# Kernel tuning notes

Hardware: AMD Instinct MI355X
Metric: run time of the kernel (lower is better)

The kernel has to match this reference:

```python
import jax, jax.numpy as jnp
import numpy as np

HEADS = 8
DIM_HEAD = 64
QUERY_DIM = 512
CONTEXT_DIM = 768
INNER_DIM = HEADS * DIM_HEAD  # 512
SCALE = DIM_HEAD ** -0.5


def setup_inputs() -> dict:
    key = jax.random.key(0)
    ks = jax.random.split(key, 7)
    B, N, M = 4, 2048, 1024
    x = jax.random.normal(ks[0], (B, N, QUERY_DIM), dtype=jnp.float32)
    context = jax.random.normal(ks[1], (B, M, CONTEXT_DIM), dtype=jnp.float32)
    # torch Linear weights stored as (out_features, in_features); y = x @ W.T
    Wq = jax.random.normal(ks[2], (INNER_DIM, QUERY_DIM), dtype=jnp.float32) * (QUERY_DIM ** -0.5)
    Wk = jax.random.normal(ks[3], (INNER_DIM, CONTEXT_DIM), dtype=jnp.float32) * (CONTEXT_DIM ** -0.5)
    Wv = jax.random.normal(ks[4], (INNER_DIM, CONTEXT_DIM), dtype=jnp.float32) * (CONTEXT_DIM ** -0.5)
    Wo = jax.random.normal(ks[5], (QUERY_DIM, INNER_DIM), dtype=jnp.float32) * (INNER_DIM ** -0.5)
    bo = jax.random.normal(ks[6], (QUERY_DIM,), dtype=jnp.float32) * 0.01
    return {"x": x, "context": context, "Wq": Wq, "Wk": Wk, "Wv": Wv, "Wo": Wo, "bo": bo}


def reference(x, context, Wq, Wk, Wv, Wo, bo):
    B, N, _ = x.shape
    M = context.shape[1]
    h, d = HEADS, DIM_HEAD
    q = jnp.einsum('bnc,ic->bni', x, Wq)        # [B,N,inner]
    k = jnp.einsum('bmc,ic->bmi', context, Wk)  # [B,M,inner]
    v = jnp.einsum('bmc,ic->bmi', context, Wv)  # [B,M,inner]
    # split heads: b n (h d) -> b h n d
    q = q.reshape(B, N, h, d).transpose(0, 2, 1, 3)
    k = k.reshape(B, M, h, d).transpose(0, 2, 1, 3)
    v = v.reshape(B, M, h, d).transpose(0, 2, 1, 3)
    # fp32 upcast for QK^T (inputs already fp32; kept explicit for fidelity)
    sim = jnp.einsum('bhnd,bhmd->bhnm', q.astype(jnp.float32), k.astype(jnp.float32)) * SCALE
    attn = jax.nn.softmax(sim, axis=-1)
    out = jnp.einsum('bhnm,bhmd->bhnd', attn, v)  # [B,h,N,d]
    out = out.transpose(0, 2, 1, 3).reshape(B, N, h * d)  # b n (h d)
    return jnp.einsum('bni,oi->bno', out, Wo) + bo  # dropout p=0 in eval
```

## Files before the change

### kernel.cpp

```cpp
#include <hip/hip_runtime.h>

using u16 = unsigned short;
typedef __bf16 bf16x8 __attribute__((ext_vector_type(8)));
typedef __bf16 bf16x2 __attribute__((ext_vector_type(2)));
typedef float  f32x4  __attribute__((ext_vector_type(4)));
typedef float  f32x16 __attribute__((ext_vector_type(16)));

#define MFMA16x16x32 __builtin_amdgcn_mfma_f32_16x16x32_bf16
#define MFMA32x32x16 __builtin_amdgcn_mfma_f32_32x32x16_bf16

#if __has_builtin(__builtin_amdgcn_exp2f)
#define EXP2 __builtin_amdgcn_exp2f
#else
#define EXP2 exp2f
#endif

static __device__ __forceinline__ unsigned f2bf_u(float f){
  unsigned x = __builtin_bit_cast(unsigned, f);
  return (x + 0x7fffu + ((x >> 16) & 1u)) >> 16;
}

static __device__ __forceinline__ void gll16(const void* g, void* l){
  __builtin_amdgcn_global_load_lds((const __attribute__((address_space(1))) void*)g,
                                   (__attribute__((address_space(3))) void*)l, 16, 0, 0);
}

static __device__ __forceinline__ f32x16 splat16(float x){
  f32x16 v;
#pragma unroll
  for (int i = 0; i < 16; ++i) v[i] = x;
  return v;
}

__global__ void __launch_bounds__(256) cvt_all(
    const float* __restrict__ x,  u16* __restrict__ xb,
    const float* __restrict__ cx, u16* __restrict__ cxb,
    const float* __restrict__ wq, u16* __restrict__ wqb,
    const float* __restrict__ wk, u16* __restrict__ wkb,
    const float* __restrict__ wv, u16* __restrict__ wvb,
    const float* __restrict__ wo, u16* __restrict__ wob)
{
  const float* in; u16* out; int n4;
  switch (blockIdx.y){
    case 0: in=x;  out=xb;  n4=(4*2048*512)/4; break;
    case 1: in=cx; out=cxb; n4=(4*1024*768)/4; break;
    case 2: in=wq; out=wqb; n4=(512*512)/4;    break;
    case 3: in=wk; out=wkb; n4=(512*768)/4;    break;
    case 4: in=wv; out=wvb; n4=(512*768)/4;    break;
    default:in=wo; out=wob; n4=(512*512)/4;    break;
  }
  int i = blockIdx.x*256 + threadIdx.x;
  const int stride = gridDim.x*256;
  for (; i < n4; i += stride){
    float4 f = ((const float4*)in)[i];
    ushort4 u;
    u.x = (u16)f2bf_u(f.x); u.y = (u16)f2bf_u(f.y);
    u.z = (u16)f2bf_u(f.z); u.w = (u16)f2bf_u(f.w);
    ((ushort4*)out)[i] = u;
  }
}

template<int LDA, int LDB, int KK, int OM>
static __device__ __forceinline__ void gemm_tile64(
    const u16* __restrict__ Ap, const u16* __restrict__ Bp,
    void* __restrict__ Cv, int ldc, int bx, int by,
    const float* __restrict__ bias, float scale,
    u16* __restrict__ sAp, u16* __restrict__ sBp)
{
  const int tid = threadIdx.x;
  const int w = tid >> 6, lane = tid & 63;
  const int wr = w >> 1, wc = w & 1;
  const long tm = (long)bx * 128;
  const long tn = (long)by * 64;

  f32x4 acc[4][2] = {};

  const int srl = lane >> 3, scc = lane & 7;

  auto stage = [&](int kt, int bb){
#pragma unroll
    for (int i = 0; i < 4; ++i){
      const int row = w*32 + i*8 + srl;
      const int sw = scc ^ (row & 7);
      gll16(Ap + (tm + row)*LDA + kt*64 + sw*8, sAp + bb*(128*64) + (w*32 + i*8)*64);
    }
#pragma unroll
    for (int i = 0; i < 2; ++i){
      const int row = w*16 + i*8 + srl;
      const int sw = scc ^ (row & 7);
      gll16(Bp + (tn + row)*LDB + kt*64 + sw*8, sBp + bb*(64*64) + (w*16 + i*8)*64);
    }
  };

  const int fr = lane & 15, fg = lane >> 4;
  constexpr int NK = KK / 64;

  stage(0, 0);
  __syncthreads();
  for (int kt = 0; kt < NK; ++kt){
    if (kt + 1 < NK) stage(kt + 1, (kt + 1) & 1);
    const int bb = kt & 1;
    bf16x8 af[4][2], bfr[2][2];
#pragma unroll
    for (int fm = 0; fm < 4; ++fm){
      const int row = wr*64 + fm*16 + fr;
      const int swz = row & 7;
#pragma unroll
      for (int s = 0; s < 2; ++s)
        af[fm][s] = *(const bf16x8*)&sAp[bb*(128*64) + row*64 + ((s*4 + fg) ^ swz)*8];
    }
#pragma unroll
    for (int fn = 0; fn < 2; ++fn){
      const int row = wc*32 + fn*16 + fr;
      const int swz = row & 7;
#pragma unroll
      for (int s = 0; s < 2; ++s)
        bfr[fn][s] = *(const bf16x8*)&sBp[bb*(64*64) + row*64 + ((s*4 + fg) ^ swz)*8];
    }
#pragma unroll
    for (int s = 0; s < 2; ++s)
#pragma unroll
      for (int fm = 0; fm < 4; ++fm)
#pragma unroll
        for (int fn = 0; fn < 2; ++fn)
          acc[fm][fn] = MFMA16x16x32(af[fm][s], bfr[fn][s], acc[fm][fn], 0, 0, 0);
    __syncthreads();
  }

#pragma unroll
  for (int fm = 0; fm < 4; ++fm){
#pragma unroll
    for (int fn = 0; fn < 2; ++fn){
      const long row0 = tm + wr*64 + fm*16 + fg*4;
      const long col  = tn + wc*32 + fn*16 + fr;
      if (OM == 0){
        u16* C = (u16*)Cv;
#pragma unroll
        for (int rr = 0; rr < 4; ++rr)
          C[(row0 + rr)*ldc + col] = (u16)f2bf_u(acc[fm][fn][rr] * scale);
      } else {
        float* C = (float*)Cv;
        const float bv = bias[col];
#pragma unroll
        for (int rr = 0; rr < 4; ++rr)
          C[(row0 + rr)*ldc + col] = acc[fm][fn][rr] + bv;
      }
    }
  }
}

template<int LDA, int LDB, int KK, int OM>
static __device__ __forceinline__ void gemm_tile128(
    const u16* __restrict__ Ap, const u16* __restrict__ Bp,
    void* __restrict__ Cv, int ldc, int bx, int by,
    const float* __restrict__ bias, float scale,
    u16* __restrict__ sAp, u16* __restrict__ sBp)
{
  const int tid = threadIdx.x;
  const int w = tid >> 6, lane = tid & 63;
  const int wr = w >> 1, wc = w & 1;
  const long tm = (long)bx * 128;
  const long tn = (long)by * 128;

  f32x4 acc[4][4] = {};

  const int srl = lane >> 3, scc = lane & 7;

  auto stage = [&](int kt, int bb){
#pragma unroll
    for (int i = 0; i < 4; ++i){
      const int row = w*32 + i*8 + srl;
      const int sw = scc ^ (row & 7);
      gll16(Ap + (tm + row)*LDA + kt*64 + sw*8, sAp + bb*(128*64) + (w*32 + i*8)*64);
      gll16(Bp + (tn + row)*LDB + kt*64 + sw*8, sBp + bb*(128*64) + (w*32 + i*8)*64);
    }
  };

  const int fr = lane & 15, fg = lane >> 4;
  constexpr int NK = KK / 64;

  stage(0, 0);
  __syncthreads();
  for (int kt = 0; kt < NK; ++kt){
    if (kt + 1 < NK) stage(kt + 1, (kt + 1) & 1);
    const int bb = kt & 1;
    bf16x8 af[4][2], bfr[4][2];
#pragma unroll
    for (int fm = 0; fm < 4; ++fm){
      const int row = wr*64 + fm*16 + fr;
      const int swz = row & 7;
#pragma unroll
      for (int s = 0; s < 2; ++s)
        af[fm][s] = *(const bf16x8*)&sAp[bb*(128*64) + row*64 + ((s*4 + fg) ^ swz)*8];
    }
#pragma unroll
    for (int fn = 0; fn < 4; ++fn){
      const int row = wc*64 + fn*16 + fr;
      const int swz = row & 7;
#pragma unroll
      for (int s = 0; s < 2; ++s)
        bfr[fn][s] = *(const bf16x8*)&sBp[bb*(128*64) + row*64 + ((s*4 + fg) ^ swz)*8];
    }
#pragma unroll
    for (int s = 0; s < 2; ++s)
#pragma unroll
      for (int fm = 0; fm < 4; ++fm)
#pragma unroll
        for (int fn = 0; fn < 4; ++fn)
          acc[fm][fn] = MFMA16x16x32(af[fm][s], bfr[fn][s], acc[fm][fn], 0, 0, 0);
    __syncthreads();
  }

#pragma unroll
  for (int fm = 0; fm < 4; ++fm){
#pragma unroll
    for (int fn = 0; fn < 4; ++fn){
      const long row0 = tm + wr*64 + fm*16 + fg*4;
      const long col  = tn + wc*64 + fn*16 + fr;
      if (OM == 0){
        u16* C = (u16*)Cv;
#pragma unroll
        for (int rr = 0; rr < 4; ++rr)
          C[(row0 + rr)*ldc + col] = (u16)f2bf_u(acc[fm][fn][rr] * scale);
      } else {
        float* C = (float*)Cv;
        const float bv = bias[col];
#pragma unroll
        for (int rr = 0; rr < 4; ++rr)
          C[(row0 + rr)*ldc + col] = acc[fm][fn][rr] + bv;
      }
    }
  }
}

__global__ __launch_bounds__(256, 2) void proj_fused(
    const u16* __restrict__ xb,  const u16* __restrict__ cxb,
    const u16* __restrict__ wqb, const u16* __restrict__ wkb,
    const u16* __restrict__ wvb,
    u16* __restrict__ qb, u16* __restrict__ kb, u16* __restrict__ vtb,
    float qscale)
{
  __shared__ u16 sA[2*128*64];
  __shared__ u16 sB[2*128*64];
  const int bid = blockIdx.x;
  const int lid = (bid & 7)*64 + (bid >> 3);
  if (lid < 256){
    gemm_tile128<512,512,512,0>(xb, wqb, (void*)qb, 512, lid >> 2, lid & 3,
                                nullptr, qscale, sA, sB);
  } else if (lid < 384){
    const int t = lid - 256;
    gemm_tile128<768,768,768,0>(cxb, wkb, (void*)kb, 512, t >> 2, t & 3,
                                nullptr, 1.0f, sA, sB);
  } else {
    const int t = lid - 384, z = t >> 5, r = t & 31;
    gemm_tile128<768,768,768,0>(wvb, cxb + (long)z*1024*768,
                                (void*)(vtb + (long)z*512*1024), 1024,
                                r >> 3, r & 7, nullptr, 1.0f, sA, sB);
  }
}

__global__ __launch_bounds__(256, 3) void gemm_out(
    const u16* __restrict__ ab, const u16* __restrict__ wob,
    float* __restrict__ out, const float* __restrict__ bias)
{
  __shared__ u16 sA[2*128*64];
  __shared__ u16 sB[2*64*64];
  const int bid = blockIdx.x;
  const int lid = (bid & 7)*64 + (bid >> 3);
  gemm_tile64<512,512,512,1>(ab, wob, (void*)out, 512, lid >> 3, lid & 7,
                             bias, 1.0f, sA, sB);
}

__global__ __launch_bounds__(512, 2) void attn_fwd(
    const u16* __restrict__ Q,
    const u16* __restrict__ Kb,
    const u16* __restrict__ Vt,
    u16* __restrict__ O)
{
  const int bid = blockIdx.x;
  const int lid = (bid & 7)*32 + (bid >> 3);
  const int qx = lid & 7, hh = (lid >> 3) & 7, b = lid >> 6;
  const int w = threadIdx.x >> 6, lane = threadIdx.x & 63;
  const int q31 = lane & 31, hi = lane >> 5;
  const int w4 = w & 3, kvg = w >> 2;
  const int q0 = qx*256 + w4*64;

  __shared__ u16 sK[8][64*64];
  __shared__ u16 sV[8][64*64];
  __shared__ float sLsP[16*32];
  __shared__ float sLsT[8*32];

  bf16x8 qf[2][4];
#pragma unroll
  for (int j = 0; j < 2; ++j){
    const u16* qrow = Q + (long)(b*2048 + q0 + j*32 + q31)*512 + hh*64;
#pragma unroll
    for (int ks = 0; ks < 4; ++ks)
      qf[j][ks] = *(const bf16x8*)(qrow + ks*16 + hi*8);
  }

  f32x16 o[2][2] = {{splat16(0.f), splat16(0.f)}, {splat16(0.f), splat16(0.f)}};
  float lsum0 = 0.f, lsum1 = 0.f;

  const int srl = lane >> 3, scc = lane & 7;

  auto stagePair = [&](int u){
    const int tv = 2*u + kvg;
    const int sl = tv & 7;
#pragma unroll
    for (int i = 0; i < 2; ++i){
      const int row = w4*16 + i*8 + srl;
      const int sw = scc ^ (row & 7);
      gll16(Kb + (long)(b*1024 + tv*64 + row)*512 + hh*64 + sw*8,
            &sK[sl][(w4*16 + i*8)*64]);
      gll16(Vt + (long)(b*512 + hh*64 + row)*1024 + tv*64 + sw*8,
            &sV[sl][(w4*16 + i*8)*64]);
    }
  };

  stagePair(0);
  stagePair(1);

  for (int t = 0; t < 8; ++t){
    if (t + 2 < 8) stagePair(t + 2);
    if (t <= 5)      asm volatile("s_waitcnt vmcnt(8)" ::: "memory");
    else if (t == 6) asm volatile("s_waitcnt vmcnt(4)" ::: "memory");
    else             asm volatile("s_waitcnt vmcnt(0)" ::: "memory");
    __builtin_amdgcn_s_barrier();
    asm volatile("" ::: "memory");
    const int tv = 2*t + kvg;
    const int sl = tv & 7;
    const u16* sKp = sK[sl];
    const u16* sVp = sV[sl];

#pragma unroll
    for (int mt = 0; mt < 2; ++mt){
      f32x16 s0 = splat16(-16.f), s1 = splat16(-16.f);
      const int row = mt*32 + q31;
      const int swz = row & 7;
      __builtin_amdgcn_s_setprio(1);
#pragma unroll
      for (int ks = 0; ks < 4; ++ks){
        bf16x8 kf = *(const bf16x8*)&sKp[row*64 + ((ks*2 + hi) ^ swz)*8];
        s0 = MFMA32x32x16(kf, qf[0][ks], s0, 0, 0, 0);
        s1 = MFMA32x32x16(kf, qf[1][ks], s1, 0, 0, 0);
      }
      __builtin_amdgcn_s_setprio(0);

      unsigned pk0[8], pk1[8];
#pragma unroll
      for (int r = 0; r < 16; ++r){ s0[r] = EXP2(s0[r]); lsum0 += s0[r]; }
#pragma unroll
      for (int r = 0; r < 16; ++r){ s1[r] = EXP2(s1[r]); lsum1 += s1[r]; }
#pragma unroll
      for (int p2 = 0; p2 < 8; ++p2){
        union { bf16x2 h; unsigned u; } t0, t1;
        t0.h[0] = (__bf16)s0[2*p2]; t0.h[1] = (__bf16)s0[2*p2 + 1]; pk0[p2] = t0.u;
        t1.h[0] = (__bf16)s1[2*p2]; t1.h[1] = (__bf16)s1[2*p2 + 1]; pk1[p2] = t1.u;
      }

#pragma unroll
      for (int sl2 = 0; sl2 < 2; ++sl2){
        union { unsigned u[4]; bf16x8 v; } pa0, pa1;
        {
          const unsigned ca = pk0[sl2*4 + 0], cb = pk0[sl2*4 + 1];
          const unsigned cc = pk0[sl2*4 + 2], cd = pk0[sl2*4 + 3];
          const unsigned ya = hi ? ca : cc;
          const unsigned za = (unsigned)__shfl_xor((int)ya, 32);
          const unsigned yb = hi ? cb : cd;
          const unsigned zb = (unsigned)__shfl_xor((int)yb, 32);
          pa0.u[0] = hi ? za : ca;
          pa0.u[1] = hi ? zb : cb;
          pa0.u[2] = hi ? cc : za;
          pa0.u[3] = hi ? cd : zb;
        }
        {
          const unsigned ca = pk1[sl2*4 + 0], cb = pk1[sl2*4 + 1];
          const unsigned cc = pk1[sl2*4 + 2], cd = pk1[sl2*4 + 3];
          const unsigned ya = hi ? ca : cc;
          const unsigned za = (unsigned)__shfl_xor((int)ya, 32);
          const unsigned yb = hi ? cb : cd;
          const unsigned zb = (unsigned)__shfl_xor((int)yb, 32);
          pa1.u[0] = hi ? za : ca;
          pa1.u[1] = hi ? zb : cb;
          pa1.u[2] = hi ? cc : za;
          pa1.u[3] = hi ? cd : zb;
        }
        const int s = mt*2 + sl2;
        __builtin_amdgcn_s_setprio(1);
#pragma unroll
        for (int fd = 0; fd < 2; ++fd){
          const int vrow = fd*32 + q31;
          bf16x8 bv = *(const bf16x8*)&sVp[vrow*64 + (((s*2 + hi) ^ (vrow & 7)))*8];
          o[0][fd] = MFMA32x32x16(pa0.v, bv, o[0][fd], 0, 0, 0);
          o[1][fd] = MFMA32x32x16(pa1.v, bv, o[1][fd], 0, 0, 0);
        }
        __builtin_amdgcn_s_setprio(0);
      }
    }
    asm volatile("" ::: "memory");
  }

  lsum0 += __shfl_xor(lsum0, 32);
  lsum1 += __shfl_xor(lsum1, 32);
  sLsP[(w*2 + 0)*32 + q31] = lsum0;
  sLsP[(w*2 + 1)*32 + q31] = lsum1;
  __syncthreads();

  float* sO = (float*)&sK[0][0];
  if (w >= 4){
#pragma unroll
    for (int j = 0; j < 2; ++j){
#pragma unroll
      for (int fd = 0; fd < 2; ++fd){
        float* p = sO + ((((w - 4)*2 + j)*2 + fd)*64*20) + lane*20;
#pragma unroll
        for (int k = 0; k < 4; ++k){
          f32x4 t4;
#pragma unroll
          for (int e = 0; e < 4; ++e) t4[e] = o[j][fd][4*k + e];
          *(f32x4*)(p + 4*k) = t4;
        }
      }
    }
  }
  __syncthreads();

  if (w < 4){
#pragma unroll
    for (int j = 0; j < 2; ++j){
#pragma unroll
      for (int fd = 0; fd < 2; ++fd){
        const float* p = sO + (((w*2 + j)*2 + fd)*64*20) + lane*20;
#pragma unroll
        for (int k = 0; k < 4; ++k){
          f32x4 t4 = *(const f32x4*)(p + 4*k);
#pragma unroll
          for (int e = 0; e < 4; ++e) o[j][fd][4*k + e] += t4[e];
        }
      }
    }
    const float lt0 = lsum0 + sLsP[((w + 4)*2 + 0)*32 + q31];
    const float lt1 = lsum1 + sLsP[((w + 4)*2 + 1)*32 + q31];
    sLsT[(w*2 + 0)*32 + q31] = lt0;
    sLsT[(w*2 + 1)*32 + q31] = lt1;
  }
  __syncthreads();

  if (w < 4){
#pragma unroll
    for (int j = 0; j < 2; ++j){
      f32x4 inv[4];
#pragma unroll
      for (int g = 0; g < 4; ++g){
        f32x4 ls = *(const f32x4*)&sLsT[(w*2 + j)*32 + 8*g + 4*hi];
#pragma unroll
        for (int e = 0; e < 4; ++e) inv[g][e] = 1.0f / ls[e];
      }
      u16* orow = O + (long)(b*2048 + q0 + j*32)*512 + hh*64;
#pragma unroll
      for (int fd = 0; fd < 2; ++fd){
#pragma unroll
        for (int r = 0; r < 16; ++r){
          const int q = (r & 3) + 8*(r >> 2) + 4*hi;
          const float val = o[j][fd][r] * inv[r >> 2][r & 3];
          orow[(long)q*512 + fd*32 + q31] = (u16)f2bf_u(val);
        }
      }
    }
  }
}

extern "C" void kernel_launch(void* const* d_in, const int* in_sizes, int n_in,
                              void* d_out, int out_size, void* d_ws, size_t ws_size,
                              hipStream_t stream)
{
  (void)in_sizes; (void)n_in; (void)out_size; (void)ws_size;
  const float* x   = (const float*)d_in[0];
  const float* ctx = (const float*)d_in[1];
  const float* Wq  = (const float*)d_in[2];
  const float* Wk  = (const float*)d_in[3];
  const float* Wv  = (const float*)d_in[4];
  const float* Wo  = (const float*)d_in[5];
  const float* bo  = (const float*)d_in[6];
  float* out = (float*)d_out;

  char* ws = (char*)d_ws;
  u16* xb  = (u16*)(ws + 0);
  u16* cxb = (u16*)(ws + 8388608);
  u16* wqb = (u16*)(ws + 14680064);
  u16* wkb = (u16*)(ws + 15204352);
  u16* wvb = (u16*)(ws + 15990784);
  u16* wob = (u16*)(ws + 16777216);
  u16* qb  = (u16*)(ws + 17301504);
  u16* kb  = (u16*)(ws + 25690112);
  u16* vtb = (u16*)(ws + 29884416);
  u16* ab  = (u16*)(ws + 34078720);

  cvt_all<<<dim3(1024, 6, 1), 256, 0, stream>>>(x, xb, ctx, cxb, Wq, wqb,
                                                Wk, wkb, Wv, wvb, Wo, wob);

  proj_fused<<<dim3(512, 1, 1), 256, 0, stream>>>(
      xb, cxb, wqb, wkb, wvb, qb, kb, vtb, 0.18033688011112042f);

  attn_fwd<<<dim3(256, 1, 1), 512, 0, stream>>>(qb, kb, vtb, ab);

  gemm_out<<<dim3(512, 1, 1), 256, 0, stream>>>(ab, wob, out, bo);
}
```

Baseline: 67.19 us.

## Halve attention block size to 4 waves with smaller K/V ring and more blocks

The attention kernel now uses 256-thread blocks covering 128 queries instead of 512-thread blocks covering 256, so twice as many blocks are launched. The K/V shared ring shrinks from 128 KB to 64 KB, with whole waves dedicated to loading either K or V. Prefetch depth drops from two tiles ahead to one, with a full vmcnt(0) wait each iteration. The aim is to improve occupancy and CU load balance, at the cost of doubled K/V global traffic across blocks and less latency hiding from the shallower prefetch.

```diff
diff --git a/kernel.cpp b/kernel.cpp
--- a/kernel.cpp
+++ b/kernel.cpp
@@ -271,24 +271,23 @@
                              bias, 1.0f, sA, sB);
 }
 
-__global__ __launch_bounds__(512, 2) void attn_fwd(
+__global__ __launch_bounds__(256, 2) void attn_fwd(
     const u16* __restrict__ Q,
     const u16* __restrict__ Kb,
     const u16* __restrict__ Vt,
     u16* __restrict__ O)
 {
   const int bid = blockIdx.x;
-  const int lid = (bid & 7)*32 + (bid >> 3);
-  const int qx = lid & 7, hh = (lid >> 3) & 7, b = lid >> 6;
+  const int lid = (bid & 7)*64 + (bid >> 3);
+  const int qx = lid & 15, hh = (lid >> 4) & 7, b = lid >> 7;
   const int w = threadIdx.x >> 6, lane = threadIdx.x & 63;
   const int q31 = lane & 31, hi = lane >> 5;
-  const int w4 = w & 3, kvg = w >> 2;
-  const int q0 = qx*256 + w4*64;
-
-  __shared__ u16 sK[8][64*64];
-  __shared__ u16 sV[8][64*64];
-  __shared__ float sLsP[16*32];
-  __shared__ float sLsT[8*32];
+  const int qw = w & 1, kvg = w >> 1;
+  const int q0 = qx*128 + qw*64;
+
+  __shared__ u16 sRing[8][64*64];
+  __shared__ float sLsP[8*32];
+  __shared__ float sLsT[4*32];
 
   bf16x8 qf[2][4];
 #pragma unroll
@@ -305,33 +304,39 @@
   const int srl = lane >> 3, scc = lane & 7;
 
   auto stagePair = [&](int u){
-    const int tv = 2*u + kvg;
-    const int sl = tv & 7;
-#pragma unroll
-    for (int i = 0; i < 2; ++i){
-      const int row = w4*16 + i*8 + srl;
-      const int sw = scc ^ (row & 7);
-      gll16(Kb + (long)(b*1024 + tv*64 + row)*512 + hh*64 + sw*8,
-            &sK[sl][(w4*16 + i*8)*64]);
-      gll16(Vt + (long)(b*512 + hh*64 + row)*1024 + tv*64 + sw*8,
-            &sV[sl][(w4*16 + i*8)*64]);
+    const int tvs = 2*u + (w >> 1);
+    const int sl = tvs & 3;
+    if ((w & 1) == 0){
+#pragma unroll
+      for (int i = 0; i < 8; ++i){
+        const int row = i*8 + srl;
+        const int sw = scc ^ (row & 7);
+        gll16(Kb + (long)(b*1024 + tvs*64 + row)*512 + hh*64 + sw*8,
+              &sRing[sl][(i*8)*64]);
+      }
+    } else {
+#pragma unroll
+      for (int i = 0; i < 8; ++i){
+        const int row = i*8 + srl;
+        const int sw = scc ^ (row & 7);
+        gll16(Vt + (long)(b*512 + hh*64 + row)*1024 + tvs*64 + sw*8,
+              &sRing[4 + sl][(i*8)*64]);
+      }
     }
   };
 
   stagePair(0);
-  stagePair(1);
 
   for (int t = 0; t < 8; ++t){
-    if (t + 2 < 8) stagePair(t + 2);
-    if (t <= 5)      asm volatile("s_waitcnt vmcnt(8)" ::: "memory");
-    else if (t == 6) asm volatile("s_waitcnt vmcnt(4)" ::: "memory");
-    else             asm volatile("s_waitcnt vmcnt(0)" ::: "memory");
+    asm volatile("s_waitcnt vmcnt(0)" ::: "memory");
     __builtin_amdgcn_s_barrier();
     asm volatile("" ::: "memory");
+    if (t + 1 < 8) stagePair(t + 1);
+
     const int tv = 2*t + kvg;
-    const int sl = tv & 7;
-    const u16* sKp = sK[sl];
-    const u16* sVp = sV[sl];
+    const int sl = tv & 3;
+    const u16* sKp = sRing[sl];
+    const u16* sVp = sRing[4 + sl];
 
 #pragma unroll
     for (int mt = 0; mt < 2; ++mt){
@@ -407,13 +412,13 @@
   sLsP[(w*2 + 1)*32 + q31] = lsum1;
   __syncthreads();
 
-  float* sO = (float*)&sK[0][0];
-  if (w >= 4){
+  float* sO = (float*)&sRing[0][0];
+  if (kvg == 1){
 #pragma unroll
     for (int j = 0; j < 2; ++j){
 #pragma unroll
       for (int fd = 0; fd < 2; ++fd){
-        float* p = sO + ((((w - 4)*2 + j)*2 + fd)*64*20) + lane*20;
+        float* p = sO + (((qw*2 + j)*2 + fd)*64*20) + lane*20;
 #pragma unroll
         for (int k = 0; k < 4; ++k){
           f32x4 t4;
@@ -426,12 +431,12 @@
   }
   __syncthreads();
 
-  if (w < 4){
+  if (kvg == 0){
 #pragma unroll
     for (int j = 0; j < 2; ++j){
 #pragma unroll
       for (int fd = 0; fd < 2; ++fd){
-        const float* p = sO + (((w*2 + j)*2 + fd)*64*20) + lane*20;
+        const float* p = sO + (((qw*2 + j)*2 + fd)*64*20) + lane*20;
 #pragma unroll
         for (int k = 0; k < 4; ++k){
           f32x4 t4 = *(const f32x4*)(p + 4*k);
@@ -440,20 +445,20 @@
         }
       }
     }
-    const float lt0 = lsum0 + sLsP[((w + 4)*2 + 0)*32 + q31];
-    const float lt1 = lsum1 + sLsP[((w + 4)*2 + 1)*32 + q31];
-    sLsT[(w*2 + 0)*32 + q31] = lt0;
-    sLsT[(w*2 + 1)*32 + q31] = lt1;
+    const float lt0 = lsum0 + sLsP[((2 + qw)*2 + 0)*32 + q31];
+    const float lt1 = lsum1 + sLsP[((2 + qw)*2 + 1)*32 + q31];
+    sLsT[(qw*2 + 0)*32 + q31] = lt0;
+    sLsT[(qw*2 + 1)*32 + q31] = lt1;
   }
   __syncthreads();
 
-  if (w < 4){
+  if (kvg == 0){
 #pragma unroll
     for (int j = 0; j < 2; ++j){
       f32x4 inv[4];
 #pragma unroll
       for (int g = 0; g < 4; ++g){
-        f32x4 ls = *(const f32x4*)&sLsT[(w*2 + j)*32 + 8*g + 4*hi];
+        f32x4 ls = *(const f32x4*)&sLsT[(qw*2 + j)*32 + 8*g + 4*hi];
 #pragma unroll
         for (int e = 0; e < 4; ++e) inv[g][e] = 1.0f / ls[e];
       }
@@ -503,7 +508,7 @@
   proj_fused<<<dim3(512, 1, 1), 256, 0, stream>>>(
       xb, cxb, wqb, wkb, wvb, qb, kb, vtb, 0.18033688011112042f);
 
-  attn_fwd<<<dim3(256, 1, 1), 512, 0, stream>>>(qb, kb, vtb, ab);
+  attn_fwd<<<dim3(512, 1, 1), 256, 0, stream>>>(qb, kb, vtb, ab);
 
   gemm_out<<<dim3(512, 1, 1), 256, 0, stream>>>(ab, wob, out, bo);
 }
```

Result: slower. 69.27 us (+3.1%).

## Stage 128-row KV tiles with double buffering and permlane32 swap for P

Applied to the files above, without the earlier changes.

Restructures the attention K/V staging from a 3-deep ring of 64-row tiles into double-buffered 128-row tiles (4 iterations instead of 8), with a wider 16-way swizzle for the V tile. The aim is fewer barriers and loop iterations per block. It also replaces the shfl_xor-plus-select exchange of P fragments with v_permlane32_swap, and reduces the row sums as a tree to shorten the dependency chain. The cost is a shallower prefetch with a full vmcnt(0) wait each iteration, so load latency may be less hidden.

```diff
diff --git a/kernel.cpp b/kernel.cpp
--- a/kernel.cpp
+++ b/kernel.cpp
@@ -285,8 +285,7 @@
   const int w4 = w & 3, kvg = w >> 2;
   const int q0 = qx*256 + w4*64;
 
-  __shared__ u16 sK[8][64*64];
-  __shared__ u16 sV[8][64*64];
+  __shared__ u16 sAll[8][8192];
   __shared__ float sLsP[16*32];
   __shared__ float sLsT[8*32];
 
@@ -303,38 +302,40 @@
   float lsum0 = 0.f, lsum1 = 0.f;
 
   const int srl = lane >> 3, scc = lane & 7;
-
-  auto stagePair = [&](int u){
-    const int tv = 2*u + kvg;
-    const int sl = tv & 7;
-#pragma unroll
-    for (int i = 0; i < 2; ++i){
-      const int row = w4*16 + i*8 + srl;
-      const int sw = scc ^ (row & 7);
-      gll16(Kb + (long)(b*1024 + tv*64 + row)*512 + hh*64 + sw*8,
-            &sK[sl][(w4*16 + i*8)*64]);
-      gll16(Vt + (long)(b*512 + hh*64 + row)*1024 + tv*64 + sw*8,
-            &sV[sl][(w4*16 + i*8)*64]);
+  const int vr4 = lane >> 4, vc16 = lane & 15;
+
+  auto stage = [&](int t){
+    const int tv = 2*t + kvg;
+    const int sl = t & 1;
+#pragma unroll
+    for (int i = 0; i < 4; ++i){
+      const int row = w4*32 + i*8 + srl;
+      const int cs = scc ^ (row & 7);
+      gll16(Kb + (long)(b*1024 + tv*128 + row)*512 + hh*64 + cs*8,
+            &sAll[kvg*2 + sl][(w4*32 + i*8)*64]);
+    }
+#pragma unroll
+    for (int i = 0; i < 4; ++i){
+      const int d = w4*16 + i*4 + vr4;
+      const int cs = vc16 ^ (d & 15);
+      gll16(Vt + (long)(b*512 + hh*64 + d)*1024 + tv*128 + cs*8,
+            &sAll[4 + kvg*2 + sl][(w4*16 + i*4)*128]);
     }
   };
 
-  stagePair(0);
-  stagePair(1);
-
-  for (int t = 0; t < 8; ++t){
-    if (t + 2 < 8) stagePair(t + 2);
-    if (t <= 5)      asm volatile("s_waitcnt vmcnt(8)" ::: "memory");
-    else if (t == 6) asm volatile("s_waitcnt vmcnt(4)" ::: "memory");
-    else             asm volatile("s_waitcnt vmcnt(0)" ::: "memory");
+  stage(0);
+
+  for (int t = 0; t < 4; ++t){
+    asm volatile("s_waitcnt vmcnt(0)" ::: "memory");
     __builtin_amdgcn_s_barrier();
     asm volatile("" ::: "memory");
-    const int tv = 2*t + kvg;
-    const int sl = tv & 7;
-    const u16* sKp = sK[sl];
-    const u16* sVp = sV[sl];
-
-#pragma unroll
-    for (int mt = 0; mt < 2; ++mt){
+    if (t + 1 < 4) stage(t + 1);
+
+    const u16* sKp = sAll[kvg*2 + (t & 1)];
+    const u16* sVp = sAll[4 + kvg*2 + (t & 1)];
+
+#pragma unroll
+    for (int mt = 0; mt < 4; ++mt){
       f32x16 s0 = splat16(-16.f), s1 = splat16(-16.f);
       const int row = mt*32 + q31;
       const int swz = row & 7;
@@ -347,11 +348,19 @@
       }
       __builtin_amdgcn_s_setprio(0);
 
+#pragma unroll
+      for (int r = 0; r < 16; ++r) s0[r] = EXP2(s0[r]);
+#pragma unroll
+      for (int r = 0; r < 16; ++r) s1[r] = EXP2(s1[r]);
+      {
+        float a0=s0[0]+s0[1], a1=s0[2]+s0[3], a2=s0[4]+s0[5], a3=s0[6]+s0[7];
+        float a4=s0[8]+s0[9], a5=s0[10]+s0[11], a6=s0[12]+s0[13], a7=s0[14]+s0[15];
+        lsum0 += ((a0+a1)+(a2+a3)) + ((a4+a5)+(a6+a7));
+        float c0=s1[0]+s1[1], c1=s1[2]+s1[3], c2=s1[4]+s1[5], c3=s1[6]+s1[7];
+        float c4=s1[8]+s1[9], c5=s1[10]+s1[11], c6=s1[12]+s1[13], c7=s1[14]+s1[15];
+        lsum1 += ((c0+c1)+(c2+c3)) + ((c4+c5)+(c6+c7));
+      }
       unsigned pk0[8], pk1[8];
-#pragma unroll
-      for (int r = 0; r < 16; ++r){ s0[r] = EXP2(s0[r]); lsum0 += s0[r]; }
-#pragma unroll
-      for (int r = 0; r < 16; ++r){ s1[r] = EXP2(s1[r]); lsum1 += s1[r]; }
 #pragma unroll
       for (int p2 = 0; p2 < 8; ++p2){
         union { bf16x2 h; unsigned u; } t0, t1;
@@ -363,35 +372,27 @@
       for (int sl2 = 0; sl2 < 2; ++sl2){
         union { unsigned u[4]; bf16x8 v; } pa0, pa1;
         {
-          const unsigned ca = pk0[sl2*4 + 0], cb = pk0[sl2*4 + 1];
-          const unsigned cc = pk0[sl2*4 + 2], cd = pk0[sl2*4 + 3];
-          const unsigned ya = hi ? ca : cc;
-          const unsigned za = (unsigned)__shfl_xor((int)ya, 32);
-          const unsigned yb = hi ? cb : cd;
-          const unsigned zb = (unsigned)__shfl_xor((int)yb, 32);
-          pa0.u[0] = hi ? za : ca;
-          pa0.u[1] = hi ? zb : cb;
-          pa0.u[2] = hi ? cc : za;
-          pa0.u[3] = hi ? cd : zb;
+          unsigned a = pk0[sl2*4 + 0], bq = pk0[sl2*4 + 2];
+          asm volatile("v_permlane32_swap_b32 %0, %1" : "+v"(a), "+v"(bq));
+          pa0.u[0] = a;  pa0.u[2] = bq;
+          unsigned a2 = pk0[sl2*4 + 1], b2 = pk0[sl2*4 + 3];
+          asm volatile("v_permlane32_swap_b32 %0, %1" : "+v"(a2), "+v"(b2));
+          pa0.u[1] = a2; pa0.u[3] = b2;
         }
         {
-          const unsigned ca = pk1[sl2*4 + 0], cb = pk1[sl2*4 + 1];
-          const unsigned cc = pk1[sl2*4 + 2], cd = pk1[sl2*4 + 3];
-          const unsigned ya = hi ? ca : cc;
-          const unsigned za = (unsigned)__shfl_xor((int)ya, 32);
-          const unsigned yb = hi ? cb : cd;
-          const unsigned zb = (unsigned)__shfl_xor((int)yb, 32);
-          pa1.u[0] = hi ? za : ca;
-          pa1.u[1] = hi ? zb : cb;
-          pa1.u[2] = hi ? cc : za;
-          pa1.u[3] = hi ? cd : zb;
+          unsigned a = pk1[sl2*4 + 0], bq = pk1[sl2*4 + 2];
+          asm volatile("v_permlane32_swap_b32 %0, %1" : "+v"(a), "+v"(bq));
+          pa1.u[0] = a;  pa1.u[2] = bq;
+          unsigned a2 = pk1[sl2*4 + 1], b2 = pk1[sl2*4 + 3];
+          asm volatile("v_permlane32_swap_b32 %0, %1" : "+v"(a2), "+v"(b2));
+          pa1.u[1] = a2; pa1.u[3] = b2;
         }
         const int s = mt*2 + sl2;
         __builtin_amdgcn_s_setprio(1);
 #pragma unroll
         for (int fd = 0; fd < 2; ++fd){
           const int vrow = fd*32 + q31;
-          bf16x8 bv = *(const bf16x8*)&sVp[vrow*64 + (((s*2 + hi) ^ (vrow & 7)))*8];
+          bf16x8 bv = *(const bf16x8*)&sVp[vrow*128 + (((s*2 + hi) ^ (vrow & 15)))*8];
           o[0][fd] = MFMA32x32x16(pa0.v, bv, o[0][fd], 0, 0, 0);
           o[1][fd] = MFMA32x32x16(pa1.v, bv, o[1][fd], 0, 0, 0);
         }
@@ -407,7 +408,7 @@
   sLsP[(w*2 + 1)*32 + q31] = lsum1;
   __syncthreads();
 
-  float* sO = (float*)&sK[0][0];
+  float* sO = (float*)&sAll[0][0];
   if (w >= 4){
 #pragma unroll
     for (int j = 0; j < 2; ++j){
```

After: 66.82 us. About the same (-0.5%).
